# Optimization experiments

Measured on AMD Instinct MI355X. Metric: run time of the kernel, lower is better.

## Reference

```python
import jax, jax.numpy as jnp
import numpy as np

B, C, CI, H, W = 8, 256, 128, 64, 64
EPS = 1e-5

def conv1x1(x, w, b):
    # x: [B,C,H,W], w: [O,C], b: [O]
    return jnp.einsum('bchw,oc->bohw', x, w) + b[None, :, None, None]

def avgpool2(x):
    b, c, h, w = x.shape
    return x.reshape(b, c, h // 2, 2, w // 2, 2).mean(axis=(3, 5))

def setup_inputs() -> dict:
    key = jax.random.key(0)
    ks = jax.random.split(key, 16)
    s = lambda fan: 1.0 / np.sqrt(fan)
    inp = {
        'q': jax.random.normal(ks[0], (B, C, H, W), jnp.float32),
        'k': jax.random.normal(ks[1], (B, C, H, W), jnp.float32),
        'v': jax.random.normal(ks[2], (B, C, H, W), jnp.float32),
        'Wg':  jax.random.normal(ks[3], (CI, C), jnp.float32) * s(C),
        'bg':  jax.random.normal(ks[4], (CI,), jnp.float32) * s(C),
        'Wth': jax.random.normal(ks[5], (CI, C), jnp.float32) * s(C),
        'bth': jax.random.normal(ks[6], (CI,), jnp.float32) * s(C),
        'Wph': jax.random.normal(ks[7], (CI, C), jnp.float32) * s(C),
        'bph': jax.random.normal(ks[8], (CI,), jnp.float32) * s(C),
        'Ww':  jax.random.normal(ks[9], (C, CI), jnp.float32) * s(CI),
        'bw':  jax.random.normal(ks[10], (C,), jnp.float32) * s(CI),
        'gamma': jax.random.normal(ks[11], (C,), jnp.float32) * 0.1 + 1.0,
        'beta':  jax.random.normal(ks[12], (C,), jnp.float32) * 0.1,
        'mean':  jax.random.normal(ks[13], (C,), jnp.float32) * 0.1,
        'var':   jax.random.uniform(ks[14], (C,), jnp.float32, 0.5, 1.5),
    }
    return inp

def reference(q, k, v, Wg, bg, Wth, bth, Wph, bph, Ww, bw, gamma, beta, mean, var):
    b = q.shape[0]
    # g branch on v, phi branch on q: 1x1 conv then 2x2 avg-pool (sub_sample)
    g_x = avgpool2(conv1x1(v, Wg, bg)).reshape(b, CI, -1)            # [B,CI,M]
    g_x = g_x.transpose(0, 2, 1)                                      # [B,M,CI]
    theta_x = conv1x1(k, Wth, bth).reshape(b, CI, -1).transpose(0, 2, 1)  # [B,N,CI]
    phi_x = avgpool2(conv1x1(q, Wph, bph)).reshape(b, CI, -1)        # [B,CI,M]
    f = jnp.einsum('bnc,bcm->bnm', theta_x, phi_x)                   # [B,N,M]
    f_div_C = jax.nn.softmax(f, axis=-1)
    y = jnp.einsum('bnm,bmc->bnc', f_div_C, g_x)                     # [B,N,CI]
    y = y.transpose(0, 2, 1).reshape(b, CI, H, W)
    W_y = conv1x1(y, Ww, bw)
    # BatchNorm2d (inference form)
    W_y = (W_y - mean[None, :, None, None]) * (gamma[None, :, None, None]
            * jax.lax.rsqrt(var + EPS)[None, :, None, None]) + beta[None, :, None, None]
    return W_y + v
```

## Files before the change

### kernel.cpp

```cpp
#include <hip/hip_runtime.h>
#include <cstddef>

typedef unsigned short u16;
typedef unsigned int u32;
typedef __attribute__((ext_vector_type(8))) __bf16 bf16x8;
typedef __attribute__((ext_vector_type(4))) float f32x4;

constexpr int kB = 8, kC = 256, kCI = 128, kN = 4096, kM = 1024;
constexpr float kEPS = 1e-5f;

__device__ __forceinline__ u16 f2bf(float f) {
    u32 u = __float_as_uint(f);
    u32 r = (u + 0x7fffu + ((u >> 16) & 1u)) >> 16;
    return (u16)r;
}

__global__ __launch_bounds__(256) void prep_kernel(const float* __restrict__ Wth,
                                                   const float* __restrict__ Wph,
                                                   const float* __restrict__ Wg,
                                                   const float* __restrict__ Ww,
                                                   const float* __restrict__ bw,
                                                   const float* __restrict__ gamma,
                                                   const float* __restrict__ beta,
                                                   const float* __restrict__ mean,
                                                   const float* __restrict__ var,
                                                   u16* __restrict__ Wthb,
                                                   u16* __restrict__ Wphb,
                                                   u16* __restrict__ Wgb,
                                                   u16* __restrict__ Wwsb,
                                                   float* __restrict__ bb) {
    int idx = blockIdx.x * 256 + threadIdx.x;
    if (idx < 32768) {
        Wthb[idx] = f2bf(Wth[idx]);
    } else if (idx < 65536) {
        int j = idx - 32768; Wphb[j] = f2bf(Wph[j]);
    } else if (idx < 98304) {
        int j = idx - 65536; Wgb[j] = f2bf(Wg[j]);
    } else {
        int j = idx - 98304;
        int co = j >> 7;
        float sc = gamma[co] * rsqrtf(var[co] + kEPS);
        Wwsb[j] = f2bf(Ww[j] * sc);
        if ((j & 127) == 0) bb[co] = (bw[co] - mean[co]) * sc + beta[co];
    }
}

template <int POOL>
__device__ __forceinline__ void conv_body(const float* __restrict__ x,
                                          const u16* __restrict__ Wb,
                                          const float* __restrict__ bias,
                                          u16* __restrict__ out, int Mn,
                                          int cmajor, int b, int n0) {
    __shared__ __align__(16) u16 w_lds[128 * 72];
    __shared__ __align__(16) u16 x_lds[64 * 64];
    int t = threadIdx.x;
    int w = t >> 6, lane = t & 63, l15 = lane & 15, quad = lane >> 4;
    int xn = t & 63, cbb = (t >> 6) * 2;

    f32x4 acc[8];
#pragma unroll
    for (int i = 0; i < 8; i++) acc[i] = (f32x4){0.f, 0.f, 0.f, 0.f};

    for (int c0 = 0; c0 < kC; c0 += 64) {
        __syncthreads();
#pragma unroll
        for (int i = 0; i < 4; i++) {
            int u = t + 256 * i;
            int ci = u >> 3, blk = u & 7;
            *(uint4*)&w_lds[ci * 72 + blk * 8] =
                *(const uint4*)&Wb[ci * kC + c0 + blk * 8];
        }
#pragma unroll
        for (int cc = 0; cc < 2; cc++) {
            int cb = cbb + cc;
            float f[8];
            if (POOL) {
                int p = n0 + xn, ph_ = p >> 5, pw_ = p & 31;
#pragma unroll
                for (int j = 0; j < 8; j++) {
                    const float* src = x + ((size_t)(b * kC + c0 + cb * 8 + j) * 64
                                            + 2 * ph_) * 64 + 2 * pw_;
                    float2 a = *(const float2*)src;
                    float2 b2 = *(const float2*)(src + 64);
                    f[j] = 0.25f * (a.x + a.y + b2.x + b2.y);
                }
            } else {
#pragma unroll
                for (int j = 0; j < 8; j++)
                    f[j] = x[(size_t)(b * kC + c0 + cb * 8 + j) * Mn + n0 + xn];
            }
            uint4 pk;
            pk.x = (u32)f2bf(f[0]) | ((u32)f2bf(f[1]) << 16);
            pk.y = (u32)f2bf(f[2]) | ((u32)f2bf(f[3]) << 16);
            pk.z = (u32)f2bf(f[4]) | ((u32)f2bf(f[5]) << 16);
            pk.w = (u32)f2bf(f[6]) | ((u32)f2bf(f[7]) << 16);
            *(uint4*)&x_lds[xn * 64 + ((cb ^ (xn & 7)) * 8)] = pk;
        }
        __syncthreads();

#pragma unroll
        for (int ks = 0; ks < 2; ks++) {
            int px = w * 16 + l15;
            bf16x8 xf = *(const bf16x8*)&x_lds[px * 64 + (((ks * 4 + quad) ^ (px & 7)) * 8)];
#pragma unroll
            for (int ct = 0; ct < 8; ct++) {
                bf16x8 wf = *(const bf16x8*)&w_lds[(ct * 16 + l15) * 72 + ks * 32 + quad * 8];
                if (cmajor)
                    acc[ct] = __builtin_amdgcn_mfma_f32_16x16x32_bf16(xf, wf, acc[ct], 0, 0, 0);
                else
                    acc[ct] = __builtin_amdgcn_mfma_f32_16x16x32_bf16(wf, xf, acc[ct], 0, 0, 0);
            }
        }
    }

    if (cmajor == 0) {
        int px = n0 + w * 16 + l15;
#pragma unroll
        for (int ct = 0; ct < 8; ct++) {
            int ci0 = ct * 16 + quad * 4;
            uint2 pk;
            pk.x = (u32)f2bf(acc[ct][0] + bias[ci0 + 0]) |
                   ((u32)f2bf(acc[ct][1] + bias[ci0 + 1]) << 16);
            pk.y = (u32)f2bf(acc[ct][2] + bias[ci0 + 2]) |
                   ((u32)f2bf(acc[ct][3] + bias[ci0 + 3]) << 16);
            *(uint2*)&out[(size_t)(b * Mn + px) * kCI + ci0] = pk;
        }
    } else {
        int px = n0 + w * 16 + quad * 4;
#pragma unroll
        for (int ct = 0; ct < 8; ct++) {
            int ci = ct * 16 + l15;
            float bs = bias[ci];
            uint2 pk;
            pk.x = (u32)f2bf(acc[ct][0] + bs) | ((u32)f2bf(acc[ct][1] + bs) << 16);
            pk.y = (u32)f2bf(acc[ct][2] + bs) | ((u32)f2bf(acc[ct][3] + bs) << 16);
            *(uint2*)&out[(size_t)(b * kCI + ci) * Mn + px] = pk;
        }
    }
}

__global__ __launch_bounds__(256) void convth_kernel(const float* __restrict__ x,
                                                     const u16* __restrict__ Wb,
                                                     const float* __restrict__ bias,
                                                     u16* __restrict__ out) {
    conv_body<0>(x, Wb, bias, out, kN, 0, blockIdx.y, blockIdx.x * 64);
}

__global__ __launch_bounds__(256) void convpg_kernel(const float* __restrict__ q,
                                                     const float* __restrict__ v,
                                                     const u16* __restrict__ Wph,
                                                     const u16* __restrict__ Wg,
                                                     const float* __restrict__ bph,
                                                     const float* __restrict__ bg,
                                                     u16* __restrict__ phi,
                                                     u16* __restrict__ g) {
    int z = blockIdx.z;
    conv_body<1>(z ? v : q, z ? Wg : Wph, z ? bg : bph, z ? g : phi,
                 kM, z, blockIdx.y, blockIdx.x * 64);
}

__global__ __launch_bounds__(256) void attn_kernel(const u16* __restrict__ theta,
                                                   const u16* __restrict__ phi,
                                                   const u16* __restrict__ g,
                                                   u16* __restrict__ y) {
    __shared__ __align__(16) u16 ph_lds[8192];
    __shared__ __align__(16) u16 g_lds[8192];
    __shared__ __align__(16) u16 p_lds[4096];

    int t = threadIdx.x, b = blockIdx.y, n0 = blockIdx.x * 64;
    int w = t >> 6, lane = t & 63, l15 = lane & 15, quad = lane >> 4;
    int sw = (l15 >> 1) & 3;

    bf16x8 thf[4];
    const u16* thB = theta + ((size_t)(b * kN) + n0 + w * 16 + l15) * kCI;
#pragma unroll
    for (int ks = 0; ks < 4; ks++)
        thf[ks] = *(const bf16x8*)&thB[ks * 32 + quad * 8];

    f32x4 oacc[8];
#pragma unroll
    for (int ct = 0; ct < 8; ct++) oacc[ct] = (f32x4){0.f, 0.f, 0.f, 0.f};
    float m_ = -1e30f, l_ = 0.f;

    const u16* phB = phi + (size_t)b * kM * kCI;
    const u16* gB  = g   + (size_t)b * kCI * kM;
    u16* pw = p_lds + w * 1024;

    for (int c0 = 0; c0 < kM; c0 += 64) {
        __syncthreads();
#pragma unroll
        for (int it = 0; it < 4; it++) {
            int u = t + 256 * it;
            int row = u >> 4, cb = u & 15;
            *(uint4*)&ph_lds[(cb >> 2) * 2048 + row * 32 + (((cb & 3) ^ ((row >> 1) & 3)) * 8)] =
                *(const uint4*)&phB[(size_t)(c0 + row) * kCI + cb * 8];
        }
#pragma unroll
        for (int it = 0; it < 4; it++) {
            int u = t + 256 * it;
            int ci = u >> 3, mb = u & 7;
            *(uint4*)&g_lds[(mb >> 2) * 4096 + ci * 32 + (((mb & 3) ^ ((ci >> 1) & 3)) * 8)] =
                *(const uint4*)&gB[(size_t)ci * kM + c0 + mb * 8];
        }
        __syncthreads();

        f32x4 sacc[4];
#pragma unroll
        for (int mt = 0; mt < 4; mt++) sacc[mt] = (f32x4){0.f, 0.f, 0.f, 0.f};
#pragma unroll
        for (int ks = 0; ks < 4; ks++)
#pragma unroll
            for (int mt = 0; mt < 4; mt++) {
                bf16x8 a = *(const bf16x8*)&ph_lds[ks * 2048 + (mt * 16 + l15) * 32 +
                                                   ((quad ^ sw) * 8)];
                sacc[mt] = __builtin_amdgcn_mfma_f32_16x16x32_bf16(a, thf[ks], sacc[mt], 0, 0, 0);
            }

        float mc = -1e30f;
#pragma unroll
        for (int mt = 0; mt < 4; mt++)
#pragma unroll
            for (int r = 0; r < 4; r++) mc = fmaxf(mc, sacc[mt][r]);
        mc = fmaxf(mc, __shfl_xor(mc, 16, 64));
        mc = fmaxf(mc, __shfl_xor(mc, 32, 64));
        float mn = fmaxf(m_, mc);
        int resc = __any(mn != m_);
        float alpha = __expf(m_ - mn);
        m_ = mn;
        float rs = 0.f;
#pragma unroll
        for (int mt = 0; mt < 4; mt++)
#pragma unroll
            for (int r = 0; r < 4; r++) {
                float p = __expf(sacc[mt][r] - mn);
                sacc[mt][r] = p;
                rs += p;
            }
        rs += __shfl_xor(rs, 16, 64);
        rs += __shfl_xor(rs, 32, 64);
        l_ = l_ * alpha + rs;
        if (resc) {
#pragma unroll
            for (int ct = 0; ct < 8; ct++)
#pragma unroll
                for (int r = 0; r < 4; r++) oacc[ct][r] *= alpha;
        }
#pragma unroll
        for (int mt = 0; mt < 4; mt++)
#pragma unroll
            for (int h = 0; h < 2; h++) {
                u32 d = (u32)f2bf(sacc[mt][2 * h]) | ((u32)f2bf(sacc[mt][2 * h + 1]) << 16);
                int m = mt * 16 + quad * 4 + 2 * h;
                int frag = m >> 5;
                int kblk = ((m >> 3) & 3);
                int j = (quad & 1) * 4 + 2 * h;
                *(u32*)&pw[frag * 512 + l15 * 32 + ((kblk ^ sw) * 8) + j] = d;
            }

#pragma unroll
        for (int ks2 = 0; ks2 < 2; ks2++) {
            bf16x8 bfrag = *(const bf16x8*)&pw[ks2 * 512 + l15 * 32 + ((quad ^ sw) * 8)];
#pragma unroll
            for (int ct = 0; ct < 8; ct++) {
                bf16x8 a = *(const bf16x8*)&g_lds[ks2 * 4096 + (ct * 16 + l15) * 32 +
                                                  ((quad ^ sw) * 8)];
                oacc[ct] = __builtin_amdgcn_mfma_f32_16x16x32_bf16(a, bfrag, oacc[ct], 0, 0, 0);
            }
        }
    }

    float inv = 1.0f / l_;
    int n = n0 + w * 16 + l15;
    u16* yr = y + ((size_t)(b * kN) + n) * kCI + quad * 4;
#pragma unroll
    for (int ct = 0; ct < 8; ct++) {
        uint2 pk;
        pk.x = (u32)f2bf(oacc[ct][0] * inv) | ((u32)f2bf(oacc[ct][1] * inv) << 16);
        pk.y = (u32)f2bf(oacc[ct][2] * inv) | ((u32)f2bf(oacc[ct][3] * inv) << 16);
        *(uint2*)&yr[ct * 16] = pk;
    }
}

__global__ __launch_bounds__(256) void final_kernel(const u16* __restrict__ y,
                                                    const u16* __restrict__ Wws,
                                                    const float* __restrict__ bb,
                                                    const float* __restrict__ v,
                                                    float* __restrict__ out) {
    __shared__ __align__(16) u16 y_lds[64 * 136];
    int t = threadIdx.x, b = blockIdx.y, n0 = blockIdx.x * 64;
    int w = t >> 6, lane = t & 63, l15 = lane & 15, quad = lane >> 4;

#pragma unroll
    for (int i = 0; i < 4; i++) {
        int u = t + 256 * i;
        int row = u >> 4, blk = u & 15;
        *(uint4*)&y_lds[row * 136 + blk * 8] =
            *(const uint4*)&y[(size_t)(b * kN + n0 + row) * kCI + blk * 8];
    }
    __syncthreads();

    bf16x8 af[4];
#pragma unroll
    for (int ks = 0; ks < 4; ks++)
        af[ks] = *(const bf16x8*)&y_lds[(w * 16 + l15) * 136 + ks * 32 + quad * 8];

#pragma unroll
    for (int ct = 0; ct < 16; ct++) {
        f32x4 a = (f32x4){0.f, 0.f, 0.f, 0.f};
#pragma unroll
        for (int ks = 0; ks < 4; ks++) {
            bf16x8 bf = *(const bf16x8*)&Wws[(ct * 16 + l15) * kCI + ks * 32 + quad * 8];
            a = __builtin_amdgcn_mfma_f32_16x16x32_bf16(af[ks], bf, a, 0, 0, 0);
        }
        int co = ct * 16 + l15;
        float bbv = bb[co];
        size_t base = (size_t)(b * kC + co) * kN + n0 + w * 16 + quad * 4;
        float4 vv = *(const float4*)&v[base];
        float4 ov;
        ov.x = a[0] + bbv + vv.x;
        ov.y = a[1] + bbv + vv.y;
        ov.z = a[2] + bbv + vv.z;
        ov.w = a[3] + bbv + vv.w;
        *(float4*)&out[base] = ov;
    }
}

extern "C" void kernel_launch(void* const* d_in, const int* in_sizes, int n_in,
                              void* d_out, int out_size, void* d_ws, size_t ws_size,
                              hipStream_t stream) {
    (void)in_sizes; (void)n_in; (void)out_size; (void)ws_size;
    const float* q     = (const float*)d_in[0];
    const float* k     = (const float*)d_in[1];
    const float* v     = (const float*)d_in[2];
    const float* Wg    = (const float*)d_in[3];
    const float* bg    = (const float*)d_in[4];
    const float* Wth   = (const float*)d_in[5];
    const float* bth   = (const float*)d_in[6];
    const float* Wph   = (const float*)d_in[7];
    const float* bph   = (const float*)d_in[8];
    const float* Ww    = (const float*)d_in[9];
    const float* bw    = (const float*)d_in[10];
    const float* gamma = (const float*)d_in[11];
    const float* beta  = (const float*)d_in[12];
    const float* mean  = (const float*)d_in[13];
    const float* var   = (const float*)d_in[14];
    float* out = (float*)d_out;

    u16* wsu = (u16*)d_ws;
    u16*   theta = wsu;
    u16*   phi   = theta + 4194304;
    u16*   gbuf  = phi + 1048576;
    u16*   ybuf  = gbuf + 1048576;
    u16*   Wthb  = ybuf + 4194304;
    u16*   Wphb  = Wthb + 32768;
    u16*   Wgb   = Wphb + 32768;
    u16*   Wwsb  = Wgb + 32768;
    float* bbuf  = (float*)(Wwsb + 32768);

    prep_kernel<<<dim3(512), 256, 0, stream>>>(Wth, Wph, Wg, Ww, bw, gamma, beta,
                                               mean, var, Wthb, Wphb, Wgb, Wwsb, bbuf);
    convth_kernel<<<dim3(64, 8), 256, 0, stream>>>(k, Wthb, bth, theta);
    convpg_kernel<<<dim3(16, 8, 2), 256, 0, stream>>>(q, v, Wphb, Wgb, bph, bg, phi, gbuf);
    attn_kernel<<<dim3(64, 8), 256, 0, stream>>>(theta, phi, gbuf, ybuf);
    final_kernel<<<dim3(64, 8), 256, 0, stream>>>(ybuf, Wwsb, bbuf, v, out);
}
```

Baseline: 256.0 us.

## Merge conv kernels, fold log2e into theta, lazy softmax rescale, split final

Merges the theta and phi/g 1x1 conv kernels into a single launch. The conv body now stages the whole 256-channel input tile in LDS once and reads the bf16 weights straight from global memory. Log2(e) is folded into the theta weights and bias so the attention softmax can use exp2f. The online-softmax rescale is skipped unless the running max grows by more than 8, and the row-sum shuffle reduction moves out of the loop to the end. The final projection kernel is split across two output-channel halves to double the grid. Risks include a larger LDS footprint lowering occupancy, uncached weight loads, and fp32 overflow headroom in the lazy rescale.

Result: no change. 254.9 us (-0.4%).

```diff
diff --git a/kernel.cpp b/kernel.cpp
--- a/kernel.cpp
+++ b/kernel.cpp
@@ -8,6 +8,7 @@
 
 constexpr int kB = 8, kC = 256, kCI = 128, kN = 4096, kM = 1024;
 constexpr float kEPS = 1e-5f;
+constexpr float kLOG2E = 1.44269504088896f;
 
 __device__ __forceinline__ u16 f2bf(float f) {
     u32 u = __float_as_uint(f);
@@ -16,6 +17,7 @@
 }
 
 __global__ __launch_bounds__(256) void prep_kernel(const float* __restrict__ Wth,
+                                                   const float* __restrict__ bth,
                                                    const float* __restrict__ Wph,
                                                    const float* __restrict__ Wg,
                                                    const float* __restrict__ Ww,
@@ -28,10 +30,12 @@
                                                    u16* __restrict__ Wphb,
                                                    u16* __restrict__ Wgb,
                                                    u16* __restrict__ Wwsb,
-                                                   float* __restrict__ bb) {
+                                                   float* __restrict__ bb,
+                                                   float* __restrict__ bthl) {
     int idx = blockIdx.x * 256 + threadIdx.x;
     if (idx < 32768) {
-        Wthb[idx] = f2bf(Wth[idx]);
+        Wthb[idx] = f2bf(Wth[idx] * kLOG2E);
+        if (idx < kCI) bthl[idx] = bth[idx] * kLOG2E;
     } else if (idx < 65536) {
         int j = idx - 32768; Wphb[j] = f2bf(Wph[j]);
     } else if (idx < 98304) {
@@ -50,71 +54,61 @@
                                           const u16* __restrict__ Wb,
                                           const float* __restrict__ bias,
                                           u16* __restrict__ out, int Mn,
-                                          int cmajor, int b, int n0) {
-    __shared__ __align__(16) u16 w_lds[128 * 72];
-    __shared__ __align__(16) u16 x_lds[64 * 64];
+                                          int cmajor, int b, int n0,
+                                          u16* x_lds) {
     int t = threadIdx.x;
     int w = t >> 6, lane = t & 63, l15 = lane & 15, quad = lane >> 4;
-    int xn = t & 63, cbb = (t >> 6) * 2;
+    int px = t & 63, cb8 = t >> 6;
+
+    for (int cc8 = 0; cc8 < 8; cc8++) {
+        int cb = cb8 * 8 + cc8;
+        int c0 = cb * 8;
+        float f[8];
+        if (POOL) {
+            int p = n0 + px, ph_ = p >> 5, pw_ = p & 31;
+#pragma unroll
+            for (int j = 0; j < 8; j++) {
+                const float* src = x + ((size_t)(b * kC + c0 + j) * 64
+                                        + 2 * ph_) * 64 + 2 * pw_;
+                float2 a = *(const float2*)src;
+                float2 b2 = *(const float2*)(src + 64);
+                f[j] = 0.25f * (a.x + a.y + b2.x + b2.y);
+            }
+        } else {
+#pragma unroll
+            for (int j = 0; j < 8; j++)
+                f[j] = x[(size_t)(b * kC + c0 + j) * Mn + n0 + px];
+        }
+        uint4 pk;
+        pk.x = (u32)f2bf(f[0]) | ((u32)f2bf(f[1]) << 16);
+        pk.y = (u32)f2bf(f[2]) | ((u32)f2bf(f[3]) << 16);
+        pk.z = (u32)f2bf(f[4]) | ((u32)f2bf(f[5]) << 16);
+        pk.w = (u32)f2bf(f[6]) | ((u32)f2bf(f[7]) << 16);
+        *(uint4*)&x_lds[px * 256 + ((cb ^ (px & 7)) * 8)] = pk;
+    }
+    __syncthreads();
 
     f32x4 acc[8];
 #pragma unroll
     for (int i = 0; i < 8; i++) acc[i] = (f32x4){0.f, 0.f, 0.f, 0.f};
 
-    for (int c0 = 0; c0 < kC; c0 += 64) {
-        __syncthreads();
-#pragma unroll
-        for (int i = 0; i < 4; i++) {
-            int u = t + 256 * i;
-            int ci = u >> 3, blk = u & 7;
-            *(uint4*)&w_lds[ci * 72 + blk * 8] =
-                *(const uint4*)&Wb[ci * kC + c0 + blk * 8];
-        }
-#pragma unroll
-        for (int cc = 0; cc < 2; cc++) {
-            int cb = cbb + cc;
-            float f[8];
-            if (POOL) {
-                int p = n0 + xn, ph_ = p >> 5, pw_ = p & 31;
-#pragma unroll
-                for (int j = 0; j < 8; j++) {
-                    const float* src = x + ((size_t)(b * kC + c0 + cb * 8 + j) * 64
-                                            + 2 * ph_) * 64 + 2 * pw_;
-                    float2 a = *(const float2*)src;
-                    float2 b2 = *(const float2*)(src + 64);
-                    f[j] = 0.25f * (a.x + a.y + b2.x + b2.y);
-                }
-            } else {
-#pragma unroll
-                for (int j = 0; j < 8; j++)
-                    f[j] = x[(size_t)(b * kC + c0 + cb * 8 + j) * Mn + n0 + xn];
-            }
-            uint4 pk;
-            pk.x = (u32)f2bf(f[0]) | ((u32)f2bf(f[1]) << 16);
-            pk.y = (u32)f2bf(f[2]) | ((u32)f2bf(f[3]) << 16);
-            pk.z = (u32)f2bf(f[4]) | ((u32)f2bf(f[5]) << 16);
-            pk.w = (u32)f2bf(f[6]) | ((u32)f2bf(f[7]) << 16);
-            *(uint4*)&x_lds[xn * 64 + ((cb ^ (xn & 7)) * 8)] = pk;
-        }
-        __syncthreads();
-
-#pragma unroll
-        for (int ks = 0; ks < 2; ks++) {
-            int px = w * 16 + l15;
-            bf16x8 xf = *(const bf16x8*)&x_lds[px * 64 + (((ks * 4 + quad) ^ (px & 7)) * 8)];
-#pragma unroll
-            for (int ct = 0; ct < 8; ct++) {
-                bf16x8 wf = *(const bf16x8*)&w_lds[(ct * 16 + l15) * 72 + ks * 32 + quad * 8];
-                if (cmajor)
-                    acc[ct] = __builtin_amdgcn_mfma_f32_16x16x32_bf16(xf, wf, acc[ct], 0, 0, 0);
-                else
-                    acc[ct] = __builtin_amdgcn_mfma_f32_16x16x32_bf16(wf, xf, acc[ct], 0, 0, 0);
-            }
+    int rpx = w * 16 + l15;
+#pragma unroll
+    for (int ks = 0; ks < 8; ks++) {
+        bf16x8 xf = *(const bf16x8*)&x_lds[rpx * 256 +
+                                           (((ks * 4 + quad) ^ (rpx & 7)) * 8)];
+#pragma unroll
+        for (int ct = 0; ct < 8; ct++) {
+            bf16x8 wf = *(const bf16x8*)&Wb[(ct * 16 + l15) * kC + ks * 32 + quad * 8];
+            if (cmajor)
+                acc[ct] = __builtin_amdgcn_mfma_f32_16x16x32_bf16(xf, wf, acc[ct], 0, 0, 0);
+            else
+                acc[ct] = __builtin_amdgcn_mfma_f32_16x16x32_bf16(wf, xf, acc[ct], 0, 0, 0);
         }
     }
 
     if (cmajor == 0) {
-        int px = n0 + w * 16 + l15;
+        int opx = n0 + w * 16 + l15;
 #pragma unroll
         for (int ct = 0; ct < 8; ct++) {
             int ci0 = ct * 16 + quad * 4;
@@ -123,10 +117,10 @@
                    ((u32)f2bf(acc[ct][1] + bias[ci0 + 1]) << 16);
             pk.y = (u32)f2bf(acc[ct][2] + bias[ci0 + 2]) |
                    ((u32)f2bf(acc[ct][3] + bias[ci0 + 3]) << 16);
-            *(uint2*)&out[(size_t)(b * Mn + px) * kCI + ci0] = pk;
+            *(uint2*)&out[(size_t)(b * Mn + opx) * kCI + ci0] = pk;
         }
     } else {
-        int px = n0 + w * 16 + quad * 4;
+        int opx = n0 + w * 16 + quad * 4;
 #pragma unroll
         for (int ct = 0; ct < 8; ct++) {
             int ci = ct * 16 + l15;
@@ -134,29 +128,33 @@
             uint2 pk;
             pk.x = (u32)f2bf(acc[ct][0] + bs) | ((u32)f2bf(acc[ct][1] + bs) << 16);
             pk.y = (u32)f2bf(acc[ct][2] + bs) | ((u32)f2bf(acc[ct][3] + bs) << 16);
-            *(uint2*)&out[(size_t)(b * kCI + ci) * Mn + px] = pk;
-        }
-    }
-}
-
-__global__ __launch_bounds__(256) void convth_kernel(const float* __restrict__ x,
-                                                     const u16* __restrict__ Wb,
-                                                     const float* __restrict__ bias,
-                                                     u16* __restrict__ out) {
-    conv_body<0>(x, Wb, bias, out, kN, 0, blockIdx.y, blockIdx.x * 64);
-}
-
-__global__ __launch_bounds__(256) void convpg_kernel(const float* __restrict__ q,
-                                                     const float* __restrict__ v,
-                                                     const u16* __restrict__ Wph,
-                                                     const u16* __restrict__ Wg,
-                                                     const float* __restrict__ bph,
-                                                     const float* __restrict__ bg,
-                                                     u16* __restrict__ phi,
-                                                     u16* __restrict__ g) {
-    int z = blockIdx.z;
-    conv_body<1>(z ? v : q, z ? Wg : Wph, z ? bg : bph, z ? g : phi,
-                 kM, z, blockIdx.y, blockIdx.x * 64);
+            *(uint2*)&out[(size_t)(b * kCI + ci) * Mn + opx] = pk;
+        }
+    }
+}
+
+__global__ __launch_bounds__(256, 4) void convs_kernel(const float* __restrict__ q,
+                                                       const float* __restrict__ k,
+                                                       const float* __restrict__ v,
+                                                       const u16* __restrict__ Wthb,
+                                                       const u16* __restrict__ Wphb,
+                                                       const u16* __restrict__ Wgb,
+                                                       const float* __restrict__ bthl,
+                                                       const float* __restrict__ bph,
+                                                       const float* __restrict__ bg,
+                                                       u16* __restrict__ theta,
+                                                       u16* __restrict__ phi,
+                                                       u16* __restrict__ g) {
+    __shared__ __align__(16) u16 x_lds[64 * 256];
+    int bx = blockIdx.x, b = blockIdx.y;
+    if (bx < 64) {
+        conv_body<0>(k, Wthb, bthl, theta, kN, 0, b, bx * 64, x_lds);
+    } else {
+        int z = (bx >= 80);
+        int n0 = (z ? (bx - 80) : (bx - 64)) * 64;
+        conv_body<1>(z ? v : q, z ? Wgb : Wphb, z ? bg : bph, z ? g : phi,
+                     kM, z, b, n0, x_lds);
+    }
 }
 
 __global__ __launch_bounds__(256) void attn_kernel(const u16* __restrict__ theta,
@@ -223,28 +221,27 @@
             for (int r = 0; r < 4; r++) mc = fmaxf(mc, sacc[mt][r]);
         mc = fmaxf(mc, __shfl_xor(mc, 16, 64));
         mc = fmaxf(mc, __shfl_xor(mc, 32, 64));
-        float mn = fmaxf(m_, mc);
-        int resc = __any(mn != m_);
-        float alpha = __expf(m_ - mn);
-        m_ = mn;
+        if (__any(mc > m_ + 8.0f)) {
+            float mn = fmaxf(m_, mc);
+            float al = exp2f(m_ - mn);
+            m_ = mn;
+            l_ *= al;
+#pragma unroll
+            for (int ct = 0; ct < 8; ct++)
+#pragma unroll
+                for (int r = 0; r < 4; r++) oacc[ct][r] *= al;
+        }
         float rs = 0.f;
 #pragma unroll
         for (int mt = 0; mt < 4; mt++)
 #pragma unroll
             for (int r = 0; r < 4; r++) {
-                float p = __expf(sacc[mt][r] - mn);
+                float p = exp2f(sacc[mt][r] - m_);
                 sacc[mt][r] = p;
                 rs += p;
             }
-        rs += __shfl_xor(rs, 16, 64);
-        rs += __shfl_xor(rs, 32, 64);
-        l_ = l_ * alpha + rs;
-        if (resc) {
-#pragma unroll
-            for (int ct = 0; ct < 8; ct++)
-#pragma unroll
-                for (int r = 0; r < 4; r++) oacc[ct][r] *= alpha;
-        }
+        l_ += rs;
+
 #pragma unroll
         for (int mt = 0; mt < 4; mt++)
 #pragma unroll
@@ -269,6 +266,8 @@
         }
     }
 
+    l_ += __shfl_xor(l_, 16, 64);
+    l_ += __shfl_xor(l_, 32, 64);
     float inv = 1.0f / l_;
     int n = n0 + w * 16 + l15;
     u16* yr = y + ((size_t)(b * kN) + n) * kCI + quad * 4;
@@ -288,6 +287,7 @@
                                                     float* __restrict__ out) {
     __shared__ __align__(16) u16 y_lds[64 * 136];
     int t = threadIdx.x, b = blockIdx.y, n0 = blockIdx.x * 64;
+    int z = blockIdx.z;
     int w = t >> 6, lane = t & 63, l15 = lane & 15, quad = lane >> 4;
 
 #pragma unroll
@@ -305,14 +305,14 @@
         af[ks] = *(const bf16x8*)&y_lds[(w * 16 + l15) * 136 + ks * 32 + quad * 8];
 
 #pragma unroll
-    for (int ct = 0; ct < 16; ct++) {
+    for (int ct = 0; ct < 8; ct++) {
+        int co = z * 128 + ct * 16 + l15;
         f32x4 a = (f32x4){0.f, 0.f, 0.f, 0.f};
 #pragma unroll
         for (int ks = 0; ks < 4; ks++) {
-            bf16x8 bf = *(const bf16x8*)&Wws[(ct * 16 + l15) * kCI + ks * 32 + quad * 8];
+            bf16x8 bf = *(const bf16x8*)&Wws[(size_t)co * kCI + ks * 32 + quad * 8];
             a = __builtin_amdgcn_mfma_f32_16x16x32_bf16(af[ks], bf, a, 0, 0, 0);
         }
-        int co = ct * 16 + l15;
         float bbv = bb[co];
         size_t base = (size_t)(b * kC + co) * kN + n0 + w * 16 + quad * 4;
         float4 vv = *(const float4*)&v[base];
@@ -356,11 +356,13 @@
     u16*   Wgb   = Wphb + 32768;
     u16*   Wwsb  = Wgb + 32768;
     float* bbuf  = (float*)(Wwsb + 32768);
-
-    prep_kernel<<<dim3(512), 256, 0, stream>>>(Wth, Wph, Wg, Ww, bw, gamma, beta,
-                                               mean, var, Wthb, Wphb, Wgb, Wwsb, bbuf);
-    convth_kernel<<<dim3(64, 8), 256, 0, stream>>>(k, Wthb, bth, theta);
-    convpg_kernel<<<dim3(16, 8, 2), 256, 0, stream>>>(q, v, Wphb, Wgb, bph, bg, phi, gbuf);
+    float* bthl  = bbuf + 256;
+
+    prep_kernel<<<dim3(512), 256, 0, stream>>>(Wth, bth, Wph, Wg, Ww, bw, gamma, beta,
+                                               mean, var, Wthb, Wphb, Wgb, Wwsb,
+                                               bbuf, bthl);
+    convs_kernel<<<dim3(96, 8), 256, 0, stream>>>(q, k, v, Wthb, Wphb, Wgb,
+                                                  bthl, bph, bg, theta, phi, gbuf);
     attn_kernel<<<dim3(64, 8), 256, 0, stream>>>(theta, phi, gbuf, ybuf);
-    final_kernel<<<dim3(64, 8), 256, 0, stream>>>(ybuf, Wwsb, bbuf, v, out);
-}
+    final_kernel<<<dim3(64, 8, 2), 256, 0, stream>>>(ybuf, Wwsb, bbuf, v, out);
+}
```
